# Performance work log

Hardware: AMD Instinct MI355X
Metric: run time of the kernel (lower is better)

Reference implementation:

```python
import jax, jax.numpy as jnp
import numpy as np

N_BINS = 15
N_SAMPLES = 2_000_000
N_CLASSES = 128


def setup_inputs() -> dict:
    key = jax.random.key(0)
    k1, k2 = jax.random.split(key)
    probs = jax.random.normal(k1, (N_SAMPLES, N_CLASSES), dtype=jnp.float32)
    labels = jax.random.randint(k2, (N_SAMPLES,), 0, N_CLASSES, dtype=jnp.int64 if jax.config.read('jax_enable_x64') else jnp.int32)
    return {"probs": probs, "labels": labels, "is_logit": 1}


def reference(probs, labels, is_logit):
    if is_logit:
        probs = jax.nn.softmax(probs, axis=-1)
    # confidences / predictions / accuracies
    confidences = jnp.max(probs, axis=1)                      # [N]
    predictions = jnp.argmax(probs, axis=1)                   # [N]
    accuracies = (predictions == labels).astype(probs.dtype)  # [N]

    # bin index for half-open bins (lower, upper]: conf in ((i)/B, (i+1)/B]
    # ceil(conf * B) - 1 maps conf==upper to bin i; clip handles conf<=0 edge.
    bin_idx = jnp.clip(jnp.ceil(confidences * N_BINS).astype(jnp.int32) - 1, 0, N_BINS - 1)

    counts = jax.ops.segment_sum(jnp.ones_like(confidences), bin_idx, num_segments=N_BINS)
    conf_sum = jax.ops.segment_sum(confidences, bin_idx, num_segments=N_BINS)
    acc_sum = jax.ops.segment_sum(accuracies, bin_idx, num_segments=N_BINS)

    n = confidences.shape[0]
    safe = jnp.maximum(counts, 1.0)
    gap = jnp.abs(conf_sum / safe - acc_sum / safe)           # [N_BINS]
    prop = counts / n                                         # [N_BINS]
    ece = jnp.sum(jnp.where(counts > 0, gap * prop, 0.0))
    return ece.reshape(1)
```

## Files before the change

### kernel.cpp

```cpp
#include <hip/hip_runtime.h>

#define N_BINS 15
#define BLOCKS 2048

__global__ __launch_bounds__(256) void ece_main(
    const float* __restrict__ probs,
    const int* __restrict__ labels,
    const int* __restrict__ is_logit_p,
    float* __restrict__ bins,
    int n_rows)
{
    __shared__ float s_count[N_BINS];
    __shared__ float s_conf[N_BINS];
    __shared__ float s_acc[N_BINS];

    const int tid = threadIdx.x;
    if (tid < N_BINS) { s_count[tid] = 0.f; s_conf[tid] = 0.f; s_acc[tid] = 0.f; }
    __syncthreads();

    const int is_logit = *is_logit_p;
    const int lane = tid & 63;
    const int wave = tid >> 6;
    const int half = lane >> 5;
    const int sub  = lane & 31;

    const long long row0   = (long long)blockIdx.x * 8 + wave * 2 + half;
    const long long stride = (long long)gridDim.x * 8;

    for (long long row = row0; row < n_rows; row += stride) {
        const float4 v = ((const float4*)(probs + (size_t)row * 128))[sub];

        float m = v.x; int mi = sub * 4;
        if (v.y > m) { m = v.y; mi = sub * 4 + 1; }
        if (v.z > m) { m = v.z; mi = sub * 4 + 2; }
        if (v.w > m) { m = v.w; mi = sub * 4 + 3; }
        #pragma unroll
        for (int off = 1; off < 32; off <<= 1) {
            float om = __shfl_xor(m, off, 64);
            int   oi = __shfl_xor(mi, off, 64);
            if (om > m || (om == m && oi < mi)) { m = om; mi = oi; }
        }

        float conf;
        if (is_logit) {
            float s = __expf(v.x - m) + __expf(v.y - m)
                    + __expf(v.z - m) + __expf(v.w - m);
            #pragma unroll
            for (int off = 1; off < 32; off <<= 1)
                s += __shfl_xor(s, off, 64);
            conf = 1.0f / s;
        } else {
            conf = m;
        }

        if (sub == 0) {
            int bin = (int)ceilf(conf * (float)N_BINS) - 1;
            bin = bin < 0 ? 0 : (bin > N_BINS - 1 ? N_BINS - 1 : bin);
            float acc = (mi == labels[row]) ? 1.0f : 0.0f;
            atomicAdd(&s_count[bin], 1.0f);
            atomicAdd(&s_conf[bin],  conf);
            atomicAdd(&s_acc[bin],   acc);
        }
    }

    __syncthreads();
    if (tid < N_BINS) {
        atomicAdd(&bins[tid],            s_count[tid]);
        atomicAdd(&bins[N_BINS + tid],   s_conf[tid]);
        atomicAdd(&bins[2*N_BINS + tid], s_acc[tid]);
    }
}

__global__ void ece_final(const float* __restrict__ bins,
                          float* __restrict__ out, int n_rows)
{
    if (threadIdx.x == 0 && blockIdx.x == 0) {
        float ece = 0.f;
        for (int i = 0; i < N_BINS; ++i) {
            float c = bins[i];
            if (c > 0.f) {
                float gap = fabsf(bins[N_BINS + i] / c - bins[2*N_BINS + i] / c);
                ece += gap * (c / (float)n_rows);
            }
        }
        out[0] = ece;
    }
}

extern "C" void kernel_launch(void* const* d_in, const int* in_sizes, int n_in,
                              void* d_out, int out_size, void* d_ws, size_t ws_size,
                              hipStream_t stream) {
    const float* probs    = (const float*)d_in[0];
    const int*   labels   = (const int*)d_in[1];
    const int*   is_logit = (const int*)d_in[2];
    float*       out      = (float*)d_out;
    float*       bins     = (float*)d_ws;
    const int n_rows = in_sizes[1];

    hipMemsetAsync(bins, 0, 3 * N_BINS * sizeof(float), stream);
    ece_main<<<BLOCKS, 256, 0, stream>>>(probs, labels, is_logit, bins, n_rows);
    ece_final<<<1, 64, 0, stream>>>(bins, out, n_rows);
}
```

Measured before the change: 1.303 ms.

## Process each row with 8 lanes and replace argmax shuffles with label ballot

Each row is now handled by 8 lanes instead of 32. Each lane loads four float4 values, so the cross-lane max and sum reductions need three shuffle steps instead of five, and every wave covers more rows at once. The index-tracking argmax is replaced by a check of whether the label's logit equals the row maximum, combined through a ballot. This removes the index shuffles and compare logic, but a tie at the maximum can count as correct where the reference argmax would pick a different index.

```diff
diff --git a/kernel.cpp b/kernel.cpp
--- a/kernel.cpp
+++ b/kernel.cpp
@@ -20,43 +20,58 @@
 
     const int is_logit = *is_logit_p;
     const int lane = tid & 63;
-    const int wave = tid >> 6;
-    const int half = lane >> 5;
-    const int sub  = lane & 31;
+    const int sub  = lane & 7;
+    const int grp  = tid >> 3;
 
-    const long long row0   = (long long)blockIdx.x * 8 + wave * 2 + half;
-    const long long stride = (long long)gridDim.x * 8;
+    long long row = (long long)blockIdx.x * 32 + grp;
+    const long long stride = (long long)gridDim.x * 32;
 
-    for (long long row = row0; row < n_rows; row += stride) {
-        const float4 v = ((const float4*)(probs + (size_t)row * 128))[sub];
+    for (; row < n_rows; row += stride) {
+        const float4* rp = (const float4*)(probs + (size_t)row * 128);
+        const float4 v0 = rp[sub];
+        const float4 v1 = rp[sub + 8];
+        const float4 v2 = rp[sub + 16];
+        const float4 v3 = rp[sub + 24];
+        const int label = labels[row];
 
-        float m = v.x; int mi = sub * 4;
-        if (v.y > m) { m = v.y; mi = sub * 4 + 1; }
-        if (v.z > m) { m = v.z; mi = sub * 4 + 2; }
-        if (v.w > m) { m = v.w; mi = sub * 4 + 3; }
-        #pragma unroll
-        for (int off = 1; off < 32; off <<= 1) {
-            float om = __shfl_xor(m, off, 64);
-            int   oi = __shfl_xor(mi, off, 64);
-            if (om > m || (om == m && oi < mi)) { m = om; mi = oi; }
-        }
+        float m = fmaxf(fmaxf(fmaxf(v0.x, v0.y), fmaxf(v0.z, v0.w)),
+                        fmaxf(fmaxf(v1.x, v1.y), fmaxf(v1.z, v1.w)));
+        m = fmaxf(m, fmaxf(fmaxf(fmaxf(v2.x, v2.y), fmaxf(v2.z, v2.w)),
+                           fmaxf(fmaxf(v3.x, v3.y), fmaxf(v3.z, v3.w))));
+        m = fmaxf(m, __shfl_xor(m, 1, 64));
+        m = fmaxf(m, __shfl_xor(m, 2, 64));
+        m = fmaxf(m, __shfl_xor(m, 4, 64));
 
         float conf;
         if (is_logit) {
-            float s = __expf(v.x - m) + __expf(v.y - m)
-                    + __expf(v.z - m) + __expf(v.w - m);
-            #pragma unroll
-            for (int off = 1; off < 32; off <<= 1)
-                s += __shfl_xor(s, off, 64);
+            float s = __expf(v0.x - m) + __expf(v0.y - m)
+                    + __expf(v0.z - m) + __expf(v0.w - m)
+                    + __expf(v1.x - m) + __expf(v1.y - m)
+                    + __expf(v1.z - m) + __expf(v1.w - m)
+                    + __expf(v2.x - m) + __expf(v2.y - m)
+                    + __expf(v2.z - m) + __expf(v2.w - m)
+                    + __expf(v3.x - m) + __expf(v3.y - m)
+                    + __expf(v3.z - m) + __expf(v3.w - m);
+            s += __shfl_xor(s, 1, 64);
+            s += __shfl_xor(s, 2, 64);
+            s += __shfl_xor(s, 4, 64);
             conf = 1.0f / s;
         } else {
             conf = m;
         }
 
+        const int f = label >> 2;
+        const int c = label & 3;
+        const int k = f >> 3;
+        float4 vk = (k == 0) ? v0 : (k == 1) ? v1 : (k == 2) ? v2 : v3;
+        float lv = (c == 0) ? vk.x : (c == 1) ? vk.y : (c == 2) ? vk.z : vk.w;
+        const bool mine = ((f & 7) == sub) && (lv == m);
+        const unsigned long long bal = __ballot(mine);
+
         if (sub == 0) {
             int bin = (int)ceilf(conf * (float)N_BINS) - 1;
             bin = bin < 0 ? 0 : (bin > N_BINS - 1 ? N_BINS - 1 : bin);
-            float acc = (mi == labels[row]) ? 1.0f : 0.0f;
+            const float acc = ((bal >> (lane & 56)) & 0xFFull) ? 1.0f : 0.0f;
             atomicAdd(&s_count[bin], 1.0f);
             atomicAdd(&s_conf[bin],  conf);
             atomicAdd(&s_acc[bin],   acc);
```

Measured after the change: 1.281 ms. Within noise of the previous version (-1.7%).
